# Kernel optimization log

Hardware: AMD Instinct MI355X
Metric: run time of the kernel (lower is better)

The kernel has to match this reference:

```python
import jax, jax.numpy as jnp
import numpy as np

B, T, V, E, H, D = 2048, 50, 65, 100, 20, 5  # batch, block, vocab, n_embd, heads, head_size


def setup_inputs() -> dict:
    key = jax.random.key(0)
    ks = jax.random.split(key, 12)
    idx = jax.random.randint(ks[0], (B, T), 0, V)
    targets = jax.random.randint(ks[1], (B, T), 0, V)
    tok_emb = jax.random.normal(ks[2], (V, E), dtype=jnp.float32) * 0.02
    pos_emb = jax.random.normal(ks[3], (T, E), dtype=jnp.float32) * 0.02
    # per-head Linear(N_EMBD, head_size, bias=False) weights, stacked over heads: [H, D, E]
    Wk = jax.random.normal(ks[4], (H, D, E), dtype=jnp.float32) * 0.1
    Wq = jax.random.normal(ks[5], (H, D, E), dtype=jnp.float32) * 0.1
    Wv = jax.random.normal(ks[6], (H, D, E), dtype=jnp.float32) * 0.1
    W_ff = jax.random.normal(ks[7], (E, E), dtype=jnp.float32) * 0.1
    b_ff = jnp.zeros((E,), dtype=jnp.float32)
    W_lm = jax.random.normal(ks[8], (V, E), dtype=jnp.float32) * 0.1
    b_lm = jnp.zeros((V,), dtype=jnp.float32)
    return {"idx": idx, "targets": targets, "tok_emb": tok_emb, "pos_emb": pos_emb,
            "Wk": Wk, "Wq": Wq, "Wv": Wv, "W_ff": W_ff, "b_ff": b_ff,
            "W_lm": W_lm, "b_lm": b_lm}


def reference(idx, targets, tok_emb, pos_emb, Wk, Wq, Wv, W_ff, b_ff, W_lm, b_lm):
    Bs, Ts = idx.shape
    x = tok_emb[idx] + pos_emb[:Ts]  # [B, T, E]
    # batched over all heads (equivalent to the per-head Python loop + concat)
    k = jnp.einsum('bte,hde->bhtd', x, Wk)
    q = jnp.einsum('bte,hde->bhtd', x, Wq)
    v = jnp.einsum('bte,hde->bhtd', x, Wv)
    # NOTE: faithful to original: k @ q^T, scaled by C**0.5 (multiply, C = N_EMBD)
    scale = jnp.asarray(E, x.dtype) ** 0.5
    w = jnp.einsum('bhtd,bhsd->bhts', k, q) * scale  # [B, H, T, S]
    tril = jnp.tril(jnp.ones((Ts, Ts), dtype=bool))
    w = jnp.where(tril, w, -jnp.inf)
    # original: torch.softmax(weights, dim=1) on [B, T, S] -> axis 't' here (axis=2)
    w = jax.nn.softmax(w, axis=2)
    attn = jnp.einsum('bhts,bhsd->bhtd', w, v)
    attn = attn.transpose(0, 2, 1, 3).reshape(Bs, Ts, H * D)  # concat heads -> [B, T, E]
    h = jax.nn.relu(attn @ W_ff.T + b_ff)  # FeedForward applied AFTER attention
    logits = h @ W_lm.T + b_lm  # [B, T, V]
    logits2d = logits.reshape(Bs * Ts, V)
    tflat = targets.reshape(Bs * Ts)
    logp = jax.nn.log_softmax(logits2d, axis=-1)
    loss = -jnp.take_along_axis(logp, tflat[:, None], axis=-1).mean()
    return (logits2d, loss)
```

## Files before the change

### kernel.cpp

```cpp
#include <hip/hip_runtime.h>
#include <hip/hip_bf16.h>

#define Bb 2048
#define Tt 50
#define Vv 65
#define Ee 100
#define Hh 20
#define Dd 5

typedef __bf16 v8bf __attribute__((ext_vector_type(8)));
typedef short v8s __attribute__((ext_vector_type(8)));
typedef short v4s __attribute__((ext_vector_type(4)));
typedef float f32x4 __attribute__((ext_vector_type(4)));

__device__ __forceinline__ v8bf bzero8() {
    v8s z = {0, 0, 0, 0, 0, 0, 0, 0};
    union { v8s s; v8bf b; } u; u.s = z; return u.b;
}
__device__ __forceinline__ unsigned short bfbits(float f) {
    union { __hip_bfloat16 h; unsigned short s; } c;
    c.h = __float2bfloat16(f);
    return c.s;
}
__device__ __forceinline__ float bf2f(short s) {
    union { unsigned i; float f; } c; c.i = ((unsigned)(unsigned short)s) << 16; return c.f;
}
__device__ __forceinline__ unsigned pack2(float a, float b) {
    return (unsigned)bfbits(a) | ((unsigned)bfbits(b) << 16);
}

__device__ __forceinline__ f32x4 mfma_16x16x16_bf16(v4s a, v4s b, f32x4 c) {
#if __has_builtin(__builtin_amdgcn_mfma_f32_16x16x16bf16_1k)
    return __builtin_amdgcn_mfma_f32_16x16x16bf16_1k(a, b, c, 0, 0, 0);
#else
    f32x4 d;
    asm volatile("v_mfma_f32_16x16x16_bf16 %0, %1, %2, %3\n\ts_nop 7\n\ts_nop 4"
                 : "=v"(d) : "v"(a), "v"(b), "v"(c));
    return d;
#endif
}

#define WS_WKQV 1024
#define WS_WFF  (1024 + 81920)
#define WS_WLM  (1024 + 81920 + 32768)
#define WS_LPART (1024 + 81920 + 32768 + 20480)

#define XSTR 136
#define R2 8000
#define R3 16000

__global__ __launch_bounds__(256) void prep_kernel(
    const float* __restrict__ Wk, const float* __restrict__ Wq,
    const float* __restrict__ Wv, const float* __restrict__ Wff,
    const float* __restrict__ Wlm, char* __restrict__ ws)
{
    int g = blockIdx.x * 256 + threadIdx.x;
    __hip_bfloat16* wkqv = (__hip_bfloat16*)(ws + WS_WKQV);
    __hip_bfloat16* wff  = (__hip_bfloat16*)(ws + WS_WFF);
    __hip_bfloat16* wlm  = (__hip_bfloat16*)(ws + WS_WLM);
    if (g < 40960) {
        int n = g >> 7, e = g & 127;
        float v = 0.f;
        if (e < Ee) {
            if (n < 100)      v = Wk[n * Ee + e] * 14.4269504089f;
            else if (n < 200) v = Wq[(n - 100) * Ee + e];
            else if (n < 300) v = Wv[(n - 200) * Ee + e];
        }
        wkqv[g] = __float2bfloat16(v);
    } else if (g < 57344) {
        int gg = g - 40960; int n = gg >> 7, e = gg & 127;
        float v = (e < Ee && n < Ee) ? Wff[n * Ee + e] : 0.f;
        wff[gg] = __float2bfloat16(v);
    } else {
        int gg = g - 57344; int n = gg >> 7, e = gg & 127;
        float v = (e < Ee && n < Vv) ? Wlm[n * Ee + e] : 0.f;
        wlm[gg] = __float2bfloat16(v);
    }
}

__global__ __launch_bounds__(256, 3) void gpt_main(
    const int* __restrict__ idx, const int* __restrict__ targets,
    const float* __restrict__ tok_emb, const float* __restrict__ pos_emb,
    const float* __restrict__ b_ff, const float* __restrict__ b_lm,
    const char* __restrict__ ws, float* __restrict__ out,
    float* __restrict__ loss_part)
{
    __shared__ __attribute__((aligned(16))) __hip_bfloat16 sh[22400];
    __shared__ int tok_s[Tt];
    __shared__ float bsum;

    const int b    = blockIdx.x;
    const int tid  = threadIdx.x;
    const int wave = tid >> 6;
    const int ln   = tid & 15;
    const int quad = (tid >> 4) & 3;

    if (tid < Tt) tok_s[tid] = idx[b * Tt + tid];
    if (tid == 0) bsum = 0.f;
    {
        const uint4 z4 = make_uint4(0u, 0u, 0u, 0u);
        for (int i = tid; i < 2800; i += 256) ((uint4*)sh)[i] = z4;
    }
    __syncthreads();
    for (int i = tid; i < Tt * 25; i += 256) {
        int r = i / 25, c4 = (i - r * 25) * 4;
        const float4 te = *(const float4*)&tok_emb[tok_s[r] * Ee + c4];
        const float4 pe = *(const float4*)&pos_emb[r * Ee + c4];
        ushort4 o;
        o.x = bfbits(te.x + pe.x); o.y = bfbits(te.y + pe.y);
        o.z = bfbits(te.z + pe.z); o.w = bfbits(te.w + pe.w);
        *(ushort4*)&sh[r * XSTR + c4] = o;
    }
    __syncthreads();

    {
        const __hip_bfloat16* wkqv = (const __hip_bfloat16*)(ws + WS_WKQV);
        f32x4 acc[5][4];
#pragma unroll
        for (int j = 0; j < 5; ++j)
#pragma unroll
            for (int mt = 0; mt < 4; ++mt) {
                f32x4 z = {0.f, 0.f, 0.f, 0.f};
                acc[j][mt] = z;
            }
#pragma unroll
        for (int kt = 0; kt < 4; ++kt) {
            v8bf a[4];
#pragma unroll
            for (int mt = 0; mt < 4; ++mt)
                a[mt] = (mt < 3 || ln < 2)
                      ? *(const v8bf*)&sh[(mt * 16 + ln) * XSTR + kt * 32 + quad * 8]
                      : bzero8();
#pragma unroll
            for (int j = 0; j < 5; ++j) {
                int nt = wave * 5 + j;
                v8bf bfr = *(const v8bf*)&wkqv[(nt * 16 + ln) * 128 + kt * 32 + quad * 8];
#pragma unroll
                for (int mt = 0; mt < 4; ++mt)
                    acc[j][mt] = __builtin_amdgcn_mfma_f32_16x16x32_bf16(a[mt], bfr, acc[j][mt], 0, 0, 0);
            }
        }
        __syncthreads();
        for (int i = tid; i < 1000; i += 256) {
            *(unsigned short*)&sh[i * 8 + 5] = 0;
            *(unsigned*)&sh[i * 8 + 6] = 0;
        }
#pragma unroll
        for (int j = 0; j < 5; ++j) {
            int n = (wave * 5 + j) * 16 + ln;
            if (n < 300) {
                int mat = n / 100;
                int jj  = n - mat * 100;
                int h   = jj / 5, d = jj - (jj / 5) * 5;
#pragma unroll
                for (int mt = 0; mt < 4; ++mt)
#pragma unroll
                    for (int r = 0; r < 4; ++r) {
                        int m = mt * 16 + quad * 4 + r;
                        if (m < Tt) {
                            __hip_bfloat16 val = __float2bfloat16(acc[j][mt][r]);
                            if (mat == 0)      sh[R2 + (h * 50 + m) * 8 + d] = val;
                            else if (mat == 1) sh[(h * 50 + m) * 8 + d] = val;
                            else               sh[R3 + (h * 5 + d) * 64 + m] = val;
                        }
                    }
            }
        }
    }
    __syncthreads();

    unsigned attp[5][8];
    {
        v4s ones4; ones4[0] = ones4[1] = ones4[2] = ones4[3] = (short)0x3F80;
#pragma unroll
        for (int hj = 0; hj < 5; ++hj) {
            const int h = wave * 5 + hj;
            v8bf qf[4], kf[4];
#pragma unroll
            for (int i = 0; i < 4; ++i) {
                int row = i * 16 + ln;
                qf[i] = (quad == 0) ? *(const v8bf*)&sh[(h * 50 + row) * 8] : bzero8();
                kf[i] = (quad == 0) ? *(const v8bf*)&sh[R2 + (h * 50 + row) * 8] : bzero8();
            }
            float rdv[4][4];
#pragma unroll
            for (int ns = 0; ns < 4; ++ns) {
                float esum[4] = {0.f, 0.f, 0.f, 0.f};
#pragma unroll
                for (int mt = ns; mt < 4; ++mt) {
                    f32x4 z = {0.f, 0.f, 0.f, 0.f};
                    f32x4 t2 = __builtin_amdgcn_mfma_f32_16x16x32_bf16(kf[mt], qf[ns], z, 0, 0, 0);
                    int s = ns * 16 + ln;
#pragma unroll
                    for (int r = 0; r < 4; ++r) {
                        int t = mt * 16 + quad * 4 + r;
                        float x = __builtin_amdgcn_exp2f(t2[r]);
                        esum[r] += (t >= s && t < Tt && s < Tt) ? x : 0.f;
                    }
                }
                v4s af;
                af[0] = (short)bfbits(esum[0]); af[1] = (short)bfbits(esum[1]);
                af[2] = (short)bfbits(esum[2]); af[3] = (short)bfbits(esum[3]);
                f32x4 z = {0.f, 0.f, 0.f, 0.f};
                f32x4 dres = mfma_16x16x16_bf16(af, ones4, z);
#pragma unroll
                for (int r = 0; r < 4; ++r) {
                    int s = ns * 16 + quad * 4 + r;
                    rdv[ns][r] = (s < Tt) ? __builtin_amdgcn_rcpf(dres[r]) : 0.f;
                }
            }
            f32x4 pac[4];
#pragma unroll
            for (int mt = 0; mt < 4; ++mt) { f32x4 z = {0.f, 0.f, 0.f, 0.f}; pac[mt] = z; }
#pragma unroll
            for (int ms = 0; ms < 4; ++ms) {
                v4s braw;
                if (ln < Dd) braw = *(const v4s*)&sh[R3 + (h * 5 + ln) * 64 + ms * 16 + quad * 4];
                else { v4s z = {0, 0, 0, 0}; braw = z; }
                v4s bvt;
#pragma unroll
                for (int j = 0; j < 4; ++j)
                    bvt[j] = (short)bfbits(bf2f(braw[j]) * rdv[ms][j]);
#pragma unroll
                for (int u = 0; u < 4 - ms; ++u) {
                    f32x4 z = {0.f, 0.f, 0.f, 0.f};
                    f32x4 t1 = __builtin_amdgcn_mfma_f32_16x16x32_bf16(qf[ms], kf[ms + u], z, 0, 0, 0);
                    int t = (ms + u) * 16 + ln;
                    v4s af;
#pragma unroll
                    for (int r = 0; r < 4; ++r) {
                        int s = ms * 16 + quad * 4 + r;
                        float x = __builtin_amdgcn_exp2f(t1[r]);
                        x = (t >= s && t < Tt && s < Tt) ? x : 0.f;
                        af[r] = (short)bfbits(x);
                    }
                    pac[ms + u] = mfma_16x16x16_bf16(af, bvt, pac[ms + u]);
                }
            }
#pragma unroll
            for (int mt = 0; mt < 4; ++mt) {
                attp[hj][mt * 2]     = pack2(pac[mt][0], pac[mt][1]);
                attp[hj][mt * 2 + 1] = pack2(pac[mt][2], pac[mt][3]);
            }
        }
    }
    __syncthreads();

#pragma unroll
    for (int hj = 0; hj < 5; ++hj) {
        int col = (wave * 5 + hj) * 5 + ln;
#pragma unroll
        for (int mt = 0; mt < 4; ++mt)
#pragma unroll
            for (int r = 0; r < 4; ++r) {
                int t = mt * 16 + quad * 4 + r;
                if (ln < Dd && t < Tt) {
                    unsigned w = attp[hj][mt * 2 + (r >> 1)];
                    unsigned short v = (unsigned short)((r & 1) ? (w >> 16) : (w & 0xffff));
                    *(unsigned short*)&sh[t * XSTR + col] = v;
                }
            }
    }
    __syncthreads();

    {
        const __hip_bfloat16* wff = (const __hip_bfloat16*)(ws + WS_WFF);
        f32x4 fac[2][4];
#pragma unroll
        for (int u = 0; u < 2; ++u)
#pragma unroll
            for (int mt = 0; mt < 4; ++mt) {
                f32x4 z = {0.f, 0.f, 0.f, 0.f};
                fac[u][mt] = z;
            }
        const int nn = (wave < 3) ? 2 : 1;
#pragma unroll
        for (int kt = 0; kt < 4; ++kt) {
            v8bf a[4];
#pragma unroll
            for (int mt = 0; mt < 4; ++mt)
                a[mt] = (mt < 3 || ln < 2)
                      ? *(const v8bf*)&sh[(mt * 16 + ln) * XSTR + kt * 32 + quad * 8]
                      : bzero8();
#pragma unroll
            for (int u = 0; u < 2; ++u) {
                if (u < nn) {
                    int nt = wave + u * 4;
                    v8bf bfr = *(const v8bf*)&wff[(nt * 16 + ln) * 128 + kt * 32 + quad * 8];
#pragma unroll
                    for (int mt = 0; mt < 4; ++mt)
                        fac[u][mt] = __builtin_amdgcn_mfma_f32_16x16x32_bf16(a[mt], bfr, fac[u][mt], 0, 0, 0);
                }
            }
        }
#pragma unroll
        for (int u = 0; u < 2; ++u) {
            if (u < nn) {
                int n = (wave + u * 4) * 16 + ln;
                if (n < Ee) {
                    float bias = b_ff[n];
#pragma unroll
                    for (int mt = 0; mt < 4; ++mt)
#pragma unroll
                        for (int r = 0; r < 4; ++r) {
                            int m = mt * 16 + quad * 4 + r;
                            if (m < Tt) {
                                float v = fac[u][mt][r] + bias;
                                sh[R2 + m * XSTR + n] = __float2bfloat16(v > 0.f ? v : 0.f);
                            }
                        }
                }
            }
        }
    }
    __syncthreads();

    {
        const __hip_bfloat16* wlm = (const __hip_bfloat16*)(ws + WS_WLM);
        float* lgl = (float*)sh;
#pragma unroll
        for (int i = 0; i < 5; ++i) {
            int job = wave + i * 4;
            int mt = job / 5, nt = job - (job / 5) * 5;
            f32x4 acc = {0.f, 0.f, 0.f, 0.f};
#pragma unroll
            for (int kt = 0; kt < 4; ++kt) {
                v8bf a = (mt < 3 || ln < 2)
                       ? *(const v8bf*)&sh[R2 + (mt * 16 + ln) * XSTR + kt * 32 + quad * 8]
                       : bzero8();
                v8bf bf = *(const v8bf*)&wlm[(nt * 16 + ln) * 128 + kt * 32 + quad * 8];
                acc = __builtin_amdgcn_mfma_f32_16x16x32_bf16(a, bf, acc, 0, 0, 0);
            }
            int n = nt * 16 + ln;
            if (n < Vv) {
                float bias = b_lm[n];
#pragma unroll
                for (int r = 0; r < 4; ++r) {
                    int m = mt * 16 + quad * 4 + r;
                    if (m < Tt) {
                        float v = acc[r] + bias;
                        out[(b * Tt + m) * Vv + n] = v;
                        lgl[m * 68 + n] = v;
                    }
                }
            }
        }
    }
    __syncthreads();

    if (tid < 200) {
        int r = tid >> 2, lv = tid & 3;
        const float* row = (const float*)sh + r * 68;
        float mx = -3.0e38f;
        for (int v = lv; v < Vv; v += 4) mx = fmaxf(mx, row[v]);
        mx = fmaxf(mx, __shfl_xor(mx, 1));
        mx = fmaxf(mx, __shfl_xor(mx, 2));
        float sum = 0.f;
        for (int v = lv; v < Vv; v += 4)
            sum += __builtin_amdgcn_exp2f((row[v] - mx) * 1.4426950408889634f);
        sum += __shfl_xor(sum, 1);
        sum += __shfl_xor(sum, 2);
        if (lv == 0) {
            float lse = mx + 0.69314718055994531f * log2f(sum);
            int tgt = targets[b * Tt + r];
            atomicAdd(&bsum, lse - row[tgt]);
        }
    }
    __syncthreads();
    if (tid == 0) loss_part[b] = bsum;
}

__global__ __launch_bounds__(256) void loss_reduce(const float* __restrict__ lp,
                                                   float* __restrict__ out)
{
    __shared__ float wsum[4];
    int tid = threadIdx.x;
    float s = 0.f;
    for (int i = tid; i < Bb; i += 256) s += lp[i];
    s += __shfl_xor(s, 1);  s += __shfl_xor(s, 2);  s += __shfl_xor(s, 4);
    s += __shfl_xor(s, 8);  s += __shfl_xor(s, 16); s += __shfl_xor(s, 32);
    if ((tid & 63) == 0) wsum[tid >> 6] = s;
    __syncthreads();
    if (tid == 0)
        out[Bb * Tt * Vv] = (wsum[0] + wsum[1] + wsum[2] + wsum[3]) * (1.0f / (float)(Bb * Tt));
}

extern "C" void kernel_launch(void* const* d_in, const int* in_sizes, int n_in,
                              void* d_out, int out_size, void* d_ws, size_t ws_size,
                              hipStream_t stream)
{
    const int* idx     = (const int*)d_in[0];
    const int* targets = (const int*)d_in[1];
    const float* tok_emb = (const float*)d_in[2];
    const float* pos_emb = (const float*)d_in[3];
    const float* Wk  = (const float*)d_in[4];
    const float* Wq  = (const float*)d_in[5];
    const float* Wv  = (const float*)d_in[6];
    const float* Wff = (const float*)d_in[7];
    const float* bff = (const float*)d_in[8];
    const float* Wlm = (const float*)d_in[9];
    const float* blm = (const float*)d_in[10];
    float* out = (float*)d_out;
    char* ws = (char*)d_ws;
    float* loss_part = (float*)(ws + WS_LPART);

    hipLaunchKernelGGL(prep_kernel, dim3(264), dim3(256), 0, stream, Wk, Wq, Wv, Wff, Wlm, ws);
    hipLaunchKernelGGL(gpt_main, dim3(Bb), dim3(256), 0, stream,
                       idx, targets, tok_emb, pos_emb, bff, blm, (const char*)ws, out, loss_part);
    hipLaunchKernelGGL(loss_reduce, dim3(1), dim3(256), 0, stream, loss_part, out);
}
```

Before: 187.4 us.

## Simplify causal masking, pack V stores, shrink LDS, fold loss reduce into atomics

Replaces per-element causal/bounds comparisons in the attention softmax with precomputed fminf mask constants applied only on diagonal and tail tiles. V is stored transposed with a tighter stride using packed 64-bit writes instead of scalar bf16 stores, which reduces shared memory. The separate loss_reduce kernel is removed: each block atomically adds its scaled partial loss into the output, which prep_kernel zeroes first. This saves one launch but changes the summation order nondeterministically.

```diff
diff --git a/kernel.cpp b/kernel.cpp
--- a/kernel.cpp
+++ b/kernel.cpp
@@ -43,18 +43,20 @@
 #define WS_WKQV 1024
 #define WS_WFF  (1024 + 81920)
 #define WS_WLM  (1024 + 81920 + 32768)
-#define WS_LPART (1024 + 81920 + 32768 + 20480)
 
 #define XSTR 136
 #define R2 8000
 #define R3 16000
+#define VSTR 52
 
 __global__ __launch_bounds__(256) void prep_kernel(
     const float* __restrict__ Wk, const float* __restrict__ Wq,
     const float* __restrict__ Wv, const float* __restrict__ Wff,
-    const float* __restrict__ Wlm, char* __restrict__ ws)
+    const float* __restrict__ Wlm, char* __restrict__ ws,
+    float* __restrict__ out)
 {
     int g = blockIdx.x * 256 + threadIdx.x;
+    if (g == 0) out[Bb * Tt * Vv] = 0.f;
     __hip_bfloat16* wkqv = (__hip_bfloat16*)(ws + WS_WKQV);
     __hip_bfloat16* wff  = (__hip_bfloat16*)(ws + WS_WFF);
     __hip_bfloat16* wlm  = (__hip_bfloat16*)(ws + WS_WLM);
@@ -82,10 +84,9 @@
     const int* __restrict__ idx, const int* __restrict__ targets,
     const float* __restrict__ tok_emb, const float* __restrict__ pos_emb,
     const float* __restrict__ b_ff, const float* __restrict__ b_lm,
-    const char* __restrict__ ws, float* __restrict__ out,
-    float* __restrict__ loss_part)
+    const char* __restrict__ ws, float* __restrict__ out)
 {
-    __shared__ __attribute__((aligned(16))) __hip_bfloat16 sh[22400];
+    __shared__ __attribute__((aligned(16))) __hip_bfloat16 sh[21200];
     __shared__ int tok_s[Tt];
     __shared__ float bsum;
 
@@ -99,7 +100,7 @@
     if (tid == 0) bsum = 0.f;
     {
         const uint4 z4 = make_uint4(0u, 0u, 0u, 0u);
-        for (int i = tid; i < 2800; i += 256) ((uint4*)sh)[i] = z4;
+        for (int i = tid; i < 2650; i += 256) ((uint4*)sh)[i] = z4;
     }
     __syncthreads();
     for (int i = tid; i < Tt * 25; i += 256) {
@@ -152,18 +153,30 @@
                 int mat = n / 100;
                 int jj  = n - mat * 100;
                 int h   = jj / 5, d = jj - (jj / 5) * 5;
-#pragma unroll
-                for (int mt = 0; mt < 4; ++mt)
-#pragma unroll
-                    for (int r = 0; r < 4; ++r) {
-                        int m = mt * 16 + quad * 4 + r;
-                        if (m < Tt) {
-                            __hip_bfloat16 val = __float2bfloat16(acc[j][mt][r]);
-                            if (mat == 0)      sh[R2 + (h * 50 + m) * 8 + d] = val;
-                            else if (mat == 1) sh[(h * 50 + m) * 8 + d] = val;
-                            else               sh[R3 + (h * 5 + d) * 64 + m] = val;
+                if (mat == 2) {
+                    int base = R3 + (h * 5 + d) * VSTR;
+#pragma unroll
+                    for (int mt = 0; mt < 4; ++mt) {
+                        if (mt < 3 || quad == 0) {
+                            float v0 = acc[j][mt][0], v1 = acc[j][mt][1];
+                            float v2 = acc[j][mt][2], v3 = acc[j][mt][3];
+                            if (mt == 3) { v2 = 0.f; v3 = 0.f; }
+                            uint2 pk = make_uint2(pack2(v0, v1), pack2(v2, v3));
+                            *(uint2*)&sh[base + mt * 16 + quad * 4] = pk;
                         }
                     }
+                } else {
+                    int roff = (mat == 0) ? R2 : 0;
+                    int rbase = h * 50;
+#pragma unroll
+                    for (int mt = 0; mt < 4; ++mt)
+#pragma unroll
+                        for (int r = 0; r < 4; ++r) {
+                            int m = mt * 16 + quad * 4 + r;
+                            if (m < Tt)
+                                sh[roff + (rbase + m) * 8 + d] = __float2bfloat16(acc[j][mt][r]);
+                        }
+                }
             }
         }
     }
@@ -171,6 +184,17 @@
 
     unsigned attp[5][8];
     {
+        const float BIGF = 3.0e38f;
+        float dA2[4], dA1[4], d50[4];
+#pragma unroll
+        for (int r = 0; r < 4; ++r) {
+            int qr = quad * 4 + r;
+            dA2[r] = (qr >= ln) ? BIGF : 0.f;
+            dA1[r] = (ln >= qr) ? BIGF : 0.f;
+            d50[r] = (qr < 2)  ? BIGF : 0.f;
+        }
+        const float tl3 = (ln < 2) ? BIGF : 0.f;
+
         v4s ones4; ones4[0] = ones4[1] = ones4[2] = ones4[3] = (short)0x3F80;
 #pragma unroll
         for (int hj = 0; hj < 5; ++hj) {
@@ -190,12 +214,12 @@
                 for (int mt = ns; mt < 4; ++mt) {
                     f32x4 z = {0.f, 0.f, 0.f, 0.f};
                     f32x4 t2 = __builtin_amdgcn_mfma_f32_16x16x32_bf16(kf[mt], qf[ns], z, 0, 0, 0);
-                    int s = ns * 16 + ln;
 #pragma unroll
                     for (int r = 0; r < 4; ++r) {
-                        int t = mt * 16 + quad * 4 + r;
                         float x = __builtin_amdgcn_exp2f(t2[r]);
-                        esum[r] += (t >= s && t < Tt && s < Tt) ? x : 0.f;
+                        if (mt == ns) x = fminf(x, dA2[r]);
+                        if (mt == 3)  x = fminf(x, d50[r]);
+                        esum[r] += x;
                     }
                 }
                 v4s af;
@@ -204,10 +228,9 @@
                 f32x4 z = {0.f, 0.f, 0.f, 0.f};
                 f32x4 dres = mfma_16x16x16_bf16(af, ones4, z);
 #pragma unroll
-                for (int r = 0; r < 4; ++r) {
-                    int s = ns * 16 + quad * 4 + r;
-                    rdv[ns][r] = (s < Tt) ? __builtin_amdgcn_rcpf(dres[r]) : 0.f;
-                }
+                for (int r = 0; r < 4; ++r)
+                    rdv[ns][r] = (ns < 3 || (quad * 4 + r) < 2)
+                               ? __builtin_amdgcn_rcpf(dres[r]) : 0.f;
             }
             f32x4 pac[4];
 #pragma unroll
@@ -215,8 +238,9 @@
 #pragma unroll
             for (int ms = 0; ms < 4; ++ms) {
                 v4s braw;
-                if (ln < Dd) braw = *(const v4s*)&sh[R3 + (h * 5 + ln) * 64 + ms * 16 + quad * 4];
-                else { v4s z = {0, 0, 0, 0}; braw = z; }
+                if (ln < Dd && (ms < 3 || quad == 0))
+                    braw = *(const v4s*)&sh[R3 + (h * 5 + ln) * VSTR + ms * 16 + quad * 4];
+                else { v4s zz = {0, 0, 0, 0}; braw = zz; }
                 v4s bvt;
 #pragma unroll
                 for (int j = 0; j < 4; ++j)
@@ -225,13 +249,13 @@
                 for (int u = 0; u < 4 - ms; ++u) {
                     f32x4 z = {0.f, 0.f, 0.f, 0.f};
                     f32x4 t1 = __builtin_amdgcn_mfma_f32_16x16x32_bf16(qf[ms], kf[ms + u], z, 0, 0, 0);
-                    int t = (ms + u) * 16 + ln;
                     v4s af;
 #pragma unroll
                     for (int r = 0; r < 4; ++r) {
-                        int s = ms * 16 + quad * 4 + r;
                         float x = __builtin_amdgcn_exp2f(t1[r]);
-                        x = (t >= s && t < Tt && s < Tt) ? x : 0.f;
+                        if (u == 0)      x = fminf(x, dA1[r]);
+                        if (ms + u == 3) x = fminf(x, tl3);
+                        if (ms == 3)     x = fminf(x, d50[r]);
                         af[r] = (short)bfbits(x);
                     }
                     pac[ms + u] = mfma_16x16x16_bf16(af, bvt, pac[ms + u]);
@@ -367,22 +391,8 @@
         }
     }
     __syncthreads();
-    if (tid == 0) loss_part[b] = bsum;
-}
-
-__global__ __launch_bounds__(256) void loss_reduce(const float* __restrict__ lp,
-                                                   float* __restrict__ out)
-{
-    __shared__ float wsum[4];
-    int tid = threadIdx.x;
-    float s = 0.f;
-    for (int i = tid; i < Bb; i += 256) s += lp[i];
-    s += __shfl_xor(s, 1);  s += __shfl_xor(s, 2);  s += __shfl_xor(s, 4);
-    s += __shfl_xor(s, 8);  s += __shfl_xor(s, 16); s += __shfl_xor(s, 32);
-    if ((tid & 63) == 0) wsum[tid >> 6] = s;
-    __syncthreads();
     if (tid == 0)
-        out[Bb * Tt * Vv] = (wsum[0] + wsum[1] + wsum[2] + wsum[3]) * (1.0f / (float)(Bb * Tt));
+        atomicAdd(&out[Bb * Tt * Vv], bsum * (1.0f / (float)(Bb * Tt)));
 }
 
 extern "C" void kernel_launch(void* const* d_in, const int* in_sizes, int n_in,
@@ -402,10 +412,8 @@
     const float* blm = (const float*)d_in[10];
     float* out = (float*)d_out;
     char* ws = (char*)d_ws;
-    float* loss_part = (float*)(ws + WS_LPART);
-
-    hipLaunchKernelGGL(prep_kernel, dim3(264), dim3(256), 0, stream, Wk, Wq, Wv, Wff, Wlm, ws);
+
+    hipLaunchKernelGGL(prep_kernel, dim3(264), dim3(256), 0, stream, Wk, Wq, Wv, Wff, Wlm, ws, out);
     hipLaunchKernelGGL(gpt_main, dim3(Bb), dim3(256), 0, stream,
-                       idx, targets, tok_emb, pos_emb, bff, blm, (const char*)ws, out, loss_part);
-    hipLaunchKernelGGL(loss_reduce, dim3(1), dim3(256), 0, stream, loss_part, out);
-}
+                       idx, targets, tok_emb, pos_emb, bff, blm, (const char*)ws, out);
+}
```

Result: faster. 177.4 us (-5.3%).
